# Optimization experiments

Measured on AMD Instinct MI355X. Metric: run time of the kernel, lower is better.

Reference implementation:

```python
import jax, jax.numpy as jnp
import numpy as np

IN_DIM = 512
HID = 256
SAMPLE = 8
TAU = 0.5
LAMBDA = 1.0
NUM_MLP = 3


def l2norm(x, axis=-1, eps=1e-12):
    n = jnp.sqrt(jnp.sum(x * x, axis=axis, keepdims=True))
    return x / jnp.maximum(n, eps)


def graphconv(adj, x, W, b):
    # GraphConv: aggregate then linear transform
    return adj @ (x @ W) + b


def mlp(x, Ws, bs):
    h = x
    for i in range(len(Ws) - 1):
        h = jax.nn.relu(h @ Ws[i] + bs[i])
    return h @ Ws[-1] + bs[-1]


def setup_inputs() -> dict:
    key = jax.random.key(0)
    ks = jax.random.split(key, 24)
    N = 16384
    # sparse-ish row-normalized adjacency surrogate (dense storage)
    a1 = jax.random.uniform(ks[0], (N, N), jnp.float32)
    a1 = (a1 > 0.999).astype(jnp.float32)
    adj1 = a1 / jnp.maximum(a1.sum(1, keepdims=True), 1.0)
    a2 = jax.random.uniform(ks[1], (N, N), jnp.float32)
    a2 = (a2 > 0.999).astype(jnp.float32)
    adj2 = a2 / jnp.maximum(a2.sum(1, keepdims=True), 1.0)
    x1 = jax.random.normal(ks[2], (N, IN_DIM), jnp.float32)
    x2 = jax.random.normal(ks[3], (N, IN_DIM), jnp.float32)
    neighbor_idx = jax.random.randint(ks[4], (N, SAMPLE), 0, N)
    neg_idx = jax.random.randint(ks[5], (N, SAMPLE), 0, N)

    def lin(k, fi, fo):
        k1, k2 = jax.random.split(k)
        s = 1.0 / np.sqrt(fi)
        return (jax.random.uniform(k1, (fi, fo), jnp.float32, -s, s),
                jax.random.uniform(k2, (fo,), jnp.float32, -s, s))

    W1, b1 = lin(ks[6], IN_DIM, HID)
    W2, b2 = lin(ks[7], HID, HID)
    tW1, tb1 = lin(ks[8], IN_DIM, HID)
    tW2, tb2 = lin(ks[9], HID, HID)
    projW, projB, semW, semB = [], [], [], []
    for i in range(NUM_MLP):
        w, b = lin(ks[10 + i], HID, HID)
        projW.append(w); projB.append(b)
        w, b = lin(ks[14 + i], HID, HID)
        semW.append(w); semB.append(b)
    return dict(adj1=adj1, adj2=adj2, x1=x1, x2=x2,
                neighbor_idx=neighbor_idx, neg_idx=neg_idx,
                W1=W1, b1=b1, W2=W2, b2=b2,
                tW1=tW1, tb1=tb1, tW2=tW2, tb2=tb2,
                projW0=projW[0], projB0=projB[0], projW1=projW[1], projB1=projB[1], projW2=projW[2], projB2=projB[2],
                semW0=semW[0], semB0=semB[0], semW1=semW[1], semB1=semB[1], semW2=semW[2], semB2=semB[2])


def contrastive_loss(projected_emd, v_emd, samp_u, samp_neg_v):
    # projected_emd, v_emd: [N,1,D]; samp_u, samp_neg_v: [N,S,D]
    pos = jnp.exp(jnp.einsum('nod,nsd->ns', projected_emd, samp_u) / TAU)  # [N,S]
    neg_sum = jnp.sum(jnp.exp(jnp.einsum('nod,nsd->ns', v_emd, samp_neg_v) / TAU), axis=1)  # [N]
    neg_score = jnp.sum(jnp.log(pos + neg_sum[:, None]), axis=1)  # [N]
    pos_score = jnp.sum(jnp.log(pos), axis=1)
    total = jnp.sum(LAMBDA * neg_score - pos_score)
    return total / samp_u.shape[0] / samp_u.shape[1]


def semi_loss(z1, z2):
    z1n = l2norm(z1); z2n = l2norm(z2)
    refl = jnp.exp((z1n @ z1n.T) / TAU)      # [N,N]
    between = jnp.exp((z1n @ z2n.T) / TAU)   # [N,N]
    return -jnp.log(jnp.diagonal(between) / (refl.sum(1) + between.sum(1) - jnp.diagonal(refl)))


def reference(adj1, adj2, x1, x2, neighbor_idx, neg_idx,
              W1, b1, W2, b2, tW1, tb1, tW2, tb2,
              projW0, projB0, projW1, projB1, projW2, projB2,
              semW0, semB0, semW1, semB1, semW2, semB2):
    pW = [projW0, projW1, projW2]; pB = [projB0, projB1, projB2]
    sW = [semW0, semW1, semW2]; sB = [semB0, semB1, semB2]
    h1 = graphconv(adj1, x1, W1, b1)
    h2 = graphconv(adj1, x2, W1, b1)
    h3 = graphconv(adj2, graphconv(adj2, x1, W1, b1), W2, b2)  # v_emd
    u_emd = l2norm(graphconv(adj2, graphconv(adj2, x1, tW1, tb1), tW2, tb2))
    projected = l2norm(mlp(h3, pW, pB))
    h1_proj = l2norm(mlp(h1, sW, sB))
    h2_proj = l2norm(mlp(h2, sW, sB))

    v_norm = l2norm(h3)
    samp_u = u_emd[neighbor_idx]          # [N,S,D]
    samp_neg_v = v_norm[neg_idx]          # [N,S,D]
    gacl = contrastive_loss(projected[:, None, :], v_norm[:, None, :], samp_u, samp_neg_v)

    l1 = semi_loss(h1_proj, h2_proj)
    l2 = semi_loss(h2_proj, h1_proj)
    sem = jnp.mean((l1 + l2) * 0.5)

    total = gacl + 0.6 * sem
    return total, gacl, sem, h3
```

## Files before the change

kernel.cpp:

```cpp
#include <hip/hip_runtime.h>
#include <hip/hip_bf16.h>

#define NN   16384
#define IND  512
#define HID  256
#define SAMP 8
#define CAP  64

typedef __bf16 bf16;
typedef __bf16 bf16x4 __attribute__((ext_vector_type(4)));
typedef __bf16 bf16x8 __attribute__((ext_vector_type(8)));
typedef float  f32x4  __attribute__((ext_vector_type(4)));

#define LOG2E_2 2.8853900817779268f

#define GLOAD_LDS16(gptr, lptr) \
  __builtin_amdgcn_global_load_lds((const __attribute__((address_space(1))) void*)(gptr), \
                                   (__attribute__((address_space(3))) void*)(lptr), 16, 0, 0)

__global__ void cvt_x(const float* __restrict__ a, bf16* __restrict__ oa,
                      const float* __restrict__ b, bf16* __restrict__ ob) {
  const float* src = blockIdx.y ? b : a;
  bf16* dst = blockIdx.y ? ob : oa;
  int stride = gridDim.x * blockDim.x;
  for (int i = blockIdx.x * blockDim.x + threadIdx.x; i < (NN * IND) / 4; i += stride) {
    float4 v = ((const float4*)src)[i];
    bf16x4 o = {(bf16)v.x, (bf16)v.y, (bf16)v.z, (bf16)v.w};
    *(bf16x4*)(dst + (size_t)i * 4) = o;
  }
}

struct WtArgs {
  const float* src[10];
  bf16* dst[10];
  int K[10];
};

__global__ void cvt_weights(WtArgs a) {
  int w = blockIdx.y;
  int K = a.K[w];
  int total = K * HID;
  const float* s = a.src[w];
  bf16* d = a.dst[w];
  for (int i = blockIdx.x * blockDim.x + threadIdx.x; i < total; i += gridDim.x * blockDim.x) {
    int k = i >> 8, n = i & 255;
    d[n * K + k] = (bf16)s[i];
  }
}

__global__ void scan_adj(const float* __restrict__ adjA, const float* __restrict__ adjB,
                         int* __restrict__ colsA, int* __restrict__ cntA,
                         int* __restrict__ colsB, int* __restrict__ cntB) {
  const float* adj = blockIdx.y ? adjB : adjA;
  int* cols = blockIdx.y ? colsB : colsA;
  int* cnt = blockIdx.y ? cntB : cntA;
  int r = blockIdx.x;
  __shared__ int c;
  if (threadIdx.x == 0) c = 0;
  __syncthreads();
  const float4* row = (const float4*)(adj + (size_t)r * NN);
  int* rc = cols + (size_t)r * CAP;
  #pragma unroll 4
  for (int i = threadIdx.x; i < NN / 4; i += 256) {
    float4 v = row[i];
    if (v.x != 0.f || v.y != 0.f || v.z != 0.f || v.w != 0.f) {
      if (v.x != 0.f) { int p = atomicAdd(&c, 1); if (p < CAP) rc[p] = 4 * i; }
      if (v.y != 0.f) { int p = atomicAdd(&c, 1); if (p < CAP) rc[p] = 4 * i + 1; }
      if (v.z != 0.f) { int p = atomicAdd(&c, 1); if (p < CAP) rc[p] = 4 * i + 2; }
      if (v.w != 0.f) { int p = atomicAdd(&c, 1); if (p < CAP) rc[p] = 4 * i + 3; }
    }
  }
  __syncthreads();
  if (threadIdx.x == 0) cnt[r] = (c < CAP) ? c : CAP;
}

struct SpmmB {
  const int* cols[4]; const int* cnt[4]; const float* X[4]; const float* bias[4];
  float* outF[4];
  bf16* outB[4];
  float* outNF[4];
};
__global__ void spmm_b(SpmmB s) {
  int j = blockIdx.y;
  int wid = threadIdx.x >> 6, lane = threadIdx.x & 63;
  int r = blockIdx.x * 4 + wid;
  int c = s.cnt[j][r];
  float val = 1.0f / (float)(c > 0 ? c : 1);
  const int* rc = s.cols[j] + (size_t)r * CAP;
  const float* X = s.X[j];
  float ax = 0.f, ay = 0.f, az = 0.f, aw = 0.f;
  for (int t = 0; t < c; ++t) {
    int col = rc[t];
    float4 v = ((const float4*)(X + (size_t)col * HID))[lane];
    ax += v.x; ay += v.y; az += v.z; aw += v.w;
  }
  float4 b4 = ((const float4*)s.bias[j])[lane];
  ax = ax * val + b4.x; ay = ay * val + b4.y; az = az * val + b4.z; aw = aw * val + b4.w;
  if (s.outF[j]) {
    float* o = s.outF[j] + (size_t)r * HID + lane * 4;
    o[0] = ax; o[1] = ay; o[2] = az; o[3] = aw;
  }
  if (s.outB[j]) {
    bf16x4 ob = {(bf16)ax, (bf16)ay, (bf16)az, (bf16)aw};
    *(bf16x4*)(s.outB[j] + (size_t)r * HID + lane * 4) = ob;
  }
  if (s.outNF[j]) {
    float ss = ax * ax + ay * ay + az * az + aw * aw;
    #pragma unroll
    for (int off = 1; off < 64; off <<= 1) ss += __shfl_xor(ss, off);
    float inv = 1.0f / fmaxf(sqrtf(ss), 1e-12f);
    float4 o = {ax * inv, ay * inv, az * inv, aw * inv};
    ((float4*)(s.outNF[j] + (size_t)r * HID))[lane] = o;
  }
}

struct GemmB {
  const bf16* A[3]; const bf16* Bt[3]; const float* bias[3];
  float* Cf[3]; bf16* Cb[3];
};
__global__ __launch_bounds__(256) void gemm_b(GemmB g, int K, int relu) {
  __shared__ bf16 As[128][64];
  __shared__ bf16 Bs[128][64];
  int j = blockIdx.z;
  const bf16* A = g.A[j];
  const bf16* Bt = g.Bt[j];
  int m0 = blockIdx.x * 128, n0 = blockIdx.y * 128;
  int tid = threadIdx.x, wid = tid >> 6, lane = tid & 63;
  int wm = wid >> 1, wn = wid & 1, q = lane >> 4, li = lane & 15;
  int r8 = lane >> 3, cc8 = lane & 7;
  int csw = cc8 ^ r8;
  f32x4 acc[4][4] = {};
  for (int k0 = 0; k0 < K; k0 += 64) {
    if (k0) __syncthreads();
    const bf16* gA = A + (size_t)(m0 + wid * 32 + r8) * K + k0 + csw * 8;
    const bf16* gB = Bt + (size_t)(n0 + wid * 32 + r8) * K + k0 + csw * 8;
    #pragma unroll
    for (int jj = 0; jj < 4; ++jj) {
      GLOAD_LDS16(gA + (size_t)jj * 8 * K, &As[wid * 32 + jj * 8][0]);
      GLOAD_LDS16(gB + (size_t)jj * 8 * K, &Bs[wid * 32 + jj * 8][0]);
    }
    __syncthreads();
    #pragma unroll
    for (int kk = 0; kk < 64; kk += 32) {
      int ca = (((q + (kk >> 3)) ^ (li & 7)) << 3);
      bf16x8 af[4], bfr[4];
      #pragma unroll
      for (int im = 0; im < 4; ++im) af[im] = *(const bf16x8*)(&As[wm * 64 + im * 16 + li][ca]);
      #pragma unroll
      for (int in = 0; in < 4; ++in) bfr[in] = *(const bf16x8*)(&Bs[wn * 64 + in * 16 + li][ca]);
      #pragma unroll
      for (int im = 0; im < 4; ++im)
        #pragma unroll
        for (int in = 0; in < 4; ++in)
          acc[im][in] = __builtin_amdgcn_mfma_f32_16x16x32_bf16(af[im], bfr[in], acc[im][in], 0, 0, 0);
    }
  }
  float* Cf = g.Cf[j];
  bf16* Cb = g.Cb[j];
  const float* bias = g.bias[j];
  #pragma unroll
  for (int im = 0; im < 4; ++im) {
    int grow0 = m0 + wm * 64 + im * 16 + q * 4;
    #pragma unroll
    for (int in = 0; in < 4; ++in) {
      int gcol = n0 + wn * 64 + in * 16 + li;
      float bv = bias ? bias[gcol] : 0.f;
      #pragma unroll
      for (int reg = 0; reg < 4; ++reg) {
        float v = acc[im][in][reg] + bv;
        if (relu) v = fmaxf(v, 0.f);
        size_t idx = (size_t)(grow0 + reg) * HID + gcol;
        if (Cf) Cf[idx] = v;
        if (Cb) Cb[idx] = (bf16)v;
      }
    }
  }
}

__global__ __launch_bounds__(128, 2) void flash_sem3(
    const bf16* __restrict__ P, const bf16* __restrict__ Q,
    float* __restrict__ Ra, float* __restrict__ Rb,
    float* __restrict__ Cr, float* __restrict__ Cc) {
  int z = blockIdx.z;
  int bid = blockIdx.y * 128 + blockIdx.x;
  int grp = bid >> 8, loc = bid & 255;
  int bx = (grp & 7) * 16 + (loc & 15);
  int by = (grp >> 3) * 16 + (loc >> 4);
  if (z < 2 && by < bx) return;
  const bf16* X = (z == 1) ? Q : P;
  const bf16* Y = (z == 0) ? P : Q;
  float* rowacc = (z == 0) ? Ra : (z == 1) ? Rb : Cr;
  float* colacc = (z == 2) ? Cc : rowacc;
  bool docol = (z == 2) || (bx != by);
  int m0 = bx * 128, n0 = by * 128;
  int wid = threadIdx.x >> 6, lane = threadIdx.x & 63;
  int q = lane >> 4, li = lane & 15;
  const bf16* Arow = X + (size_t)(m0 + wid * 64 + li) * HID + q * 8;
  const bf16* Brow = Y + (size_t)(n0 + li) * HID + q * 8;
  f32x4 acc[4][8] = {};
  #pragma unroll
  for (int kk = 0; kk < 8; ++kk) {
    bf16x8 af[4], bfr[8];
    #pragma unroll
    for (int im = 0; im < 4; ++im)
      af[im] = *(const bf16x8*)(Arow + (size_t)im * 16 * HID + kk * 32);
    #pragma unroll
    for (int in = 0; in < 8; ++in)
      bfr[in] = *(const bf16x8*)(Brow + (size_t)in * 16 * HID + kk * 32);
    #pragma unroll
    for (int im = 0; im < 4; ++im)
      #pragma unroll
      for (int in = 0; in < 8; ++in)
        acc[im][in] = __builtin_amdgcn_mfma_f32_16x16x32_bf16(af[im], bfr[in], acc[im][in], 0, 0, 0);
  }
  float cs[8] = {};
  #pragma unroll
  for (int im = 0; im < 4; ++im) {
    #pragma unroll
    for (int reg = 0; reg < 4; ++reg) {
      float rs = 0.f;
      #pragma unroll
      for (int in = 0; in < 8; ++in) {
        float e = exp2f(acc[im][in][reg] * LOG2E_2);
        rs += e;
        cs[in] += e;
      }
      rs += __shfl_xor(rs, 1); rs += __shfl_xor(rs, 2);
      rs += __shfl_xor(rs, 4); rs += __shfl_xor(rs, 8);
      if (li == 0) atomicAdd(&rowacc[m0 + wid * 64 + im * 16 + q * 4 + reg], rs);
    }
  }
  if (docol) {
    #pragma unroll
    for (int in = 0; in < 8; ++in) {
      float v = cs[in];
      v += __shfl_xor(v, 16); v += __shfl_xor(v, 32);
      if (q == 0) atomicAdd(&colacc[n0 + in * 16 + li], v);
    }
  }
}

struct NormB { const float* X[3]; float* outF[3]; bf16* outB[3]; };
__global__ void l2norm_b(NormB n) {
  int j = blockIdx.y;
  int wid = threadIdx.x >> 6, lane = threadIdx.x & 63;
  int r = blockIdx.x * 4 + wid;
  float4 a = ((const float4*)(n.X[j] + (size_t)r * HID))[lane];
  float s = a.x * a.x + a.y * a.y + a.z * a.z + a.w * a.w;
  #pragma unroll
  for (int off = 1; off < 64; off <<= 1) s += __shfl_xor(s, off);
  float inv = 1.0f / fmaxf(sqrtf(s), 1e-12f);
  a.x *= inv; a.y *= inv; a.z *= inv; a.w *= inv;
  if (n.outF[j]) ((float4*)(n.outF[j] + (size_t)r * HID))[lane] = a;
  if (n.outB[j]) {
    bf16x4 b = {(bf16)a.x, (bf16)a.y, (bf16)a.z, (bf16)a.w};
    *(bf16x4*)(n.outB[j] + (size_t)r * HID + lane * 4) = b;
  }
}

__global__ void tail_k(const float* __restrict__ proj, const float* __restrict__ vn,
                       const float* __restrict__ ue, const int* __restrict__ nbr,
                       const int* __restrict__ neg,
                       const float* __restrict__ P, const float* __restrict__ Q2,
                       const float* __restrict__ Ra, const float* __restrict__ Rb,
                       const float* __restrict__ Cr, const float* __restrict__ Cc,
                       float* __restrict__ sums) {
  int wid = threadIdx.x >> 6, lane = threadIdx.x & 63;
  int n = blockIdx.x * 4 + wid;
  if (blockIdx.y == 0) {
    float4 p = ((const float4*)(proj + (size_t)n * HID))[lane];
    float4 v = ((const float4*)(vn + (size_t)n * HID))[lane];
    float du[SAMP], dn[SAMP];
    for (int s = 0; s < SAMP; ++s) {
      int iu = nbr[n * SAMP + s];
      float4 u = ((const float4*)(ue + (size_t)iu * HID))[lane];
      float d = p.x * u.x + p.y * u.y + p.z * u.z + p.w * u.w;
      #pragma unroll
      for (int off = 1; off < 64; off <<= 1) d += __shfl_xor(d, off);
      du[s] = d;
      int iv = neg[n * SAMP + s];
      float4 w = ((const float4*)(vn + (size_t)iv * HID))[lane];
      float d2 = v.x * w.x + v.y * w.y + v.z * w.z + v.w * w.w;
      #pragma unroll
      for (int off = 1; off < 64; off <<= 1) d2 += __shfl_xor(d2, off);
      dn[s] = d2;
    }
    float negsum = 0.f;
    for (int s = 0; s < SAMP; ++s) negsum += expf(2.f * dn[s]);
    float ns = 0.f, ps = 0.f;
    for (int s = 0; s < SAMP; ++s) {
      float pl = 2.f * du[s];
      ns += logf(expf(pl) + negsum);
      ps += pl;
    }
    if (lane == 0) atomicAdd(&sums[0], ns - ps);
  } else {
    float4 a = ((const float4*)(P + (size_t)n * HID))[lane];
    float4 b = ((const float4*)(Q2 + (size_t)n * HID))[lane];
    float d = a.x * b.x + a.y * b.y + a.z * b.z + a.w * b.w;
    #pragma unroll
    for (int off = 1; off < 64; off <<= 1) d += __shfl_xor(d, off);
    float db = expf(2.f * d);
    float e2 = expf(2.f);
    float l1 = -logf(db / (Ra[n] + Cr[n] - e2));
    float l2 = -logf(db / (Rb[n] + Cc[n] - e2));
    if (lane == 0) atomicAdd(&sums[1], 0.5f * (l1 + l2));
  }
}

__global__ void final_k(const float* __restrict__ sums, float* __restrict__ out) {
  float gacl = sums[0] / (float)(NN * SAMP);
  float sem = sums[1] / (float)NN;
  out[0] = gacl + 0.6f * sem;
  out[1] = gacl;
  out[2] = sem;
}

extern "C" void kernel_launch(void* const* d_in, const int* in_sizes, int n_in,
                              void* d_out, int out_size, void* d_ws, size_t ws_size,
                              hipStream_t stream) {
  (void)in_sizes; (void)n_in; (void)out_size; (void)ws_size;
  const float* adj1 = (const float*)d_in[0];
  const float* adj2 = (const float*)d_in[1];
  const float* x1 = (const float*)d_in[2];
  const float* x2 = (const float*)d_in[3];
  const int* nbr = (const int*)d_in[4];
  const int* neg = (const int*)d_in[5];
  const float* W1 = (const float*)d_in[6];
  const float* b1 = (const float*)d_in[7];
  const float* W2 = (const float*)d_in[8];
  const float* b2 = (const float*)d_in[9];
  const float* tW1 = (const float*)d_in[10];
  const float* tb1 = (const float*)d_in[11];
  const float* tW2 = (const float*)d_in[12];
  const float* tb2 = (const float*)d_in[13];
  const float* pB[3] = {(const float*)d_in[15], (const float*)d_in[17], (const float*)d_in[19]};
  const float* sB[3] = {(const float*)d_in[21], (const float*)d_in[23], (const float*)d_in[25]};

  char* w = (char*)d_ws;
  auto alloc = [&](size_t bytes) -> char* {
    char* p = w;
    w += (bytes + 255) & ~(size_t)255;
    return p;
  };
  float* Ra = (float*)alloc((size_t)NN * 4);
  float* Rb = (float*)alloc((size_t)NN * 4);
  float* Cr = (float*)alloc((size_t)NN * 4);
  float* Cc = (float*)alloc((size_t)NN * 4);
  float* sums = (float*)alloc(256);
  size_t accBytes = (size_t)(w - (char*)d_ws);

  int* c1cols = (int*)alloc((size_t)NN * CAP * 4);
  int* c1cnt = (int*)alloc((size_t)NN * 4);
  int* c2cols = (int*)alloc((size_t)NN * CAP * 4);
  int* c2cnt = (int*)alloc((size_t)NN * 4);
  bf16* x1b = (bf16*)alloc((size_t)NN * IND * 2);
  bf16* x2b = (bf16*)alloc((size_t)NN * IND * 2);
  bf16* W1t = (bf16*)alloc((size_t)IND * HID * 2);
  bf16* tW1t = (bf16*)alloc((size_t)IND * HID * 2);
  bf16* W2t = (bf16*)alloc((size_t)HID * HID * 2);
  bf16* tW2t = (bf16*)alloc((size_t)HID * HID * 2);
  bf16* pWt[3], *sWt[3];
  for (int i = 0; i < 3; ++i) pWt[i] = (bf16*)alloc((size_t)HID * HID * 2);
  for (int i = 0; i < 3; ++i) sWt[i] = (bf16*)alloc((size_t)HID * HID * 2);
  const size_t FB = (size_t)NN * HID * 4;
  float* xw1 = (float*)alloc(FB);
  float* xw2 = (float*)alloc(FB);
  float* xt1 = (float*)alloc(FB);
  float* mlp_out = (float*)alloc(FB);
  float* projected = (float*)alloc(FB);
  float* h1p = (float*)alloc(FB);
  float* h2p = (float*)alloc(FB);
  float* v_norm = (float*)alloc(FB);
  float* gw = xw2;
  float* utw = xt1;
  float* u_emd = xw1;
  const size_t BB = (size_t)NN * HID * 2;
  bf16* h1b = (bf16*)alloc(BB);
  bf16* h2b = (bf16*)alloc(BB);
  bf16* gb = (bf16*)alloc(BB);
  bf16* h3b = (bf16*)alloc(BB);
  bf16* utb = (bf16*)alloc(BB);
  bf16* mA = (bf16*)alloc(BB);
  bf16* mB = (bf16*)alloc(BB);
  bf16* mB1 = x1b;
  bf16* mB2 = x1b + (size_t)NN * HID;
  bf16* Pb = gb;
  bf16* Qb = utb;

  hipMemsetAsync(d_ws, 0, accBytes, stream);

  WtArgs wa;
  const float* wsrc[10] = {W1, tW1, W2, tW2,
                           (const float*)d_in[14], (const float*)d_in[16], (const float*)d_in[18],
                           (const float*)d_in[20], (const float*)d_in[22], (const float*)d_in[24]};
  bf16* wdst[10] = {W1t, tW1t, W2t, tW2t, pWt[0], pWt[1], pWt[2], sWt[0], sWt[1], sWt[2]};
  int wk[10] = {IND, IND, HID, HID, HID, HID, HID, HID, HID, HID};
  for (int i = 0; i < 10; ++i) { wa.src[i] = wsrc[i]; wa.dst[i] = wdst[i]; wa.K[i] = wk[i]; }
  cvt_weights<<<dim3(512, 10), 256, 0, stream>>>(wa);
  cvt_x<<<dim3(2048, 2), 256, 0, stream>>>(x1, x1b, x2, x2b);
  scan_adj<<<dim3(NN, 2), 256, 0, stream>>>(adj1, adj2, c1cols, c1cnt, c2cols, c2cnt);

  {
    GemmB g = {};
    g.A[0] = x1b; g.Bt[0] = W1t; g.Cf[0] = xw1;
    g.A[1] = x2b; g.Bt[1] = W1t; g.Cf[1] = xw2;
    g.A[2] = x1b; g.Bt[2] = tW1t; g.Cf[2] = xt1;
    gemm_b<<<dim3(128, 2, 3), 256, 0, stream>>>(g, IND, 0);
  }
  {
    SpmmB s = {};
    s.cols[0] = c1cols; s.cnt[0] = c1cnt; s.X[0] = xw1; s.bias[0] = b1; s.outB[0] = h1b;
    s.cols[1] = c1cols; s.cnt[1] = c1cnt; s.X[1] = xw2; s.bias[1] = b1; s.outB[1] = h2b;
    s.cols[2] = c2cols; s.cnt[2] = c2cnt; s.X[2] = xw1; s.bias[2] = b1; s.outB[2] = gb;
    s.cols[3] = c2cols; s.cnt[3] = c2cnt; s.X[3] = xt1; s.bias[3] = tb1; s.outB[3] = utb;
    spmm_b<<<dim3(NN / 4, 4), 256, 0, stream>>>(s);
  }
  {
    GemmB g = {};
    g.A[0] = gb; g.Bt[0] = W2t; g.Cf[0] = gw;
    g.A[1] = utb; g.Bt[1] = tW2t; g.Cf[1] = utw;
    gemm_b<<<dim3(128, 2, 2), 256, 0, stream>>>(g, HID, 0);
  }
  float* h3out = ((float*)d_out) + 3;
  {
    SpmmB s = {};
    s.cols[0] = c2cols; s.cnt[0] = c2cnt; s.X[0] = gw; s.bias[0] = b2;
    s.outF[0] = h3out; s.outB[0] = h3b; s.outNF[0] = v_norm;
    s.cols[1] = c2cols; s.cnt[1] = c2cnt; s.X[1] = utw; s.bias[1] = tb2;
    s.outNF[1] = u_emd;
    spmm_b<<<dim3(NN / 4, 2), 256, 0, stream>>>(s);
  }
  {
    GemmB g = {};
    g.A[0] = h3b; g.Bt[0] = pWt[0]; g.bias[0] = pB[0]; g.Cb[0] = mA;
    g.A[1] = h1b; g.Bt[1] = sWt[0]; g.bias[1] = sB[0]; g.Cb[1] = gb;
    g.A[2] = h2b; g.Bt[2] = sWt[0]; g.bias[2] = sB[0]; g.Cb[2] = utb;
    gemm_b<<<dim3(128, 2, 3), 256, 0, stream>>>(g, HID, 1);
  }
  {
    GemmB g = {};
    g.A[0] = mA; g.Bt[0] = pWt[1]; g.bias[0] = pB[1]; g.Cb[0] = mB;
    g.A[1] = gb; g.Bt[1] = sWt[1]; g.bias[1] = sB[1]; g.Cb[1] = mB1;
    g.A[2] = utb; g.Bt[2] = sWt[1]; g.bias[2] = sB[1]; g.Cb[2] = mB2;
    gemm_b<<<dim3(128, 2, 3), 256, 0, stream>>>(g, HID, 1);
  }
  {
    GemmB g = {};
    g.A[0] = mB; g.Bt[0] = pWt[2]; g.bias[0] = pB[2]; g.Cf[0] = mlp_out;
    g.A[1] = mB1; g.Bt[1] = sWt[2]; g.bias[1] = sB[2]; g.Cf[1] = xw2;
    g.A[2] = mB2; g.Bt[2] = sWt[2]; g.bias[2] = sB[2]; g.Cf[2] = xt1;
    gemm_b<<<dim3(128, 2, 3), 256, 0, stream>>>(g, HID, 0);
  }
  {
    NormB nb2 = {};
    nb2.X[0] = mlp_out; nb2.outF[0] = projected;
    nb2.X[1] = xw2; nb2.outF[1] = h1p; nb2.outB[1] = Pb;
    nb2.X[2] = xt1; nb2.outF[2] = h2p; nb2.outB[2] = Qb;
    l2norm_b<<<dim3(NN / 4, 3), 256, 0, stream>>>(nb2);
  }

  flash_sem3<<<dim3(128, 128, 3), 128, 0, stream>>>(Pb, Qb, Ra, Rb, Cr, Cc);
  tail_k<<<dim3(NN / 4, 2), 256, 0, stream>>>(projected, v_norm, u_emd, nbr, neg,
                                              h1p, h2p, Ra, Rb, Cr, Cc, sums);
  final_k<<<1, 1, 0, stream>>>(sums, (float*)d_out);
}
```

Measured before the change: 3.614 ms.

## Stage sim tiles in swizzled LDS and split across four waves

The similarity/exp kernel now loads the full 128x256 A and B tiles into shared memory with direct global-to-LDS loads, using an XOR swizzle to avoid bank conflicts. Before, each wave read its operands straight from global memory, and each B row was fetched by multiple waves. The block grows to 256 threads in a 2x2 wave grid, so each wave computes a 64x64 sub-tile and holds fewer accumulators. The cost is 128KB of LDS per block, which allows one block per CU and no overlap between the load phase and the compute phase.

```diff
diff --git a/kernel.cpp b/kernel.cpp
--- a/kernel.cpp
+++ b/kernel.cpp
@@ -177,10 +177,12 @@
   }
 }
 
-__global__ __launch_bounds__(128, 2) void flash_sem3(
+__global__ __launch_bounds__(256, 1) void flash_sem4(
     const bf16* __restrict__ P, const bf16* __restrict__ Q,
     float* __restrict__ Ra, float* __restrict__ Rb,
     float* __restrict__ Cr, float* __restrict__ Cc) {
+  __shared__ bf16 As[128][256];
+  __shared__ bf16 Bs[128][256];
   int z = blockIdx.z;
   int bid = blockIdx.y * 128 + blockIdx.x;
   int grp = bid >> 8, loc = bid & 255;
@@ -193,49 +195,60 @@
   float* colacc = (z == 2) ? Cc : rowacc;
   bool docol = (z == 2) || (bx != by);
   int m0 = bx * 128, n0 = by * 128;
-  int wid = threadIdx.x >> 6, lane = threadIdx.x & 63;
-  int q = lane >> 4, li = lane & 15;
-  const bf16* Arow = X + (size_t)(m0 + wid * 64 + li) * HID + q * 8;
-  const bf16* Brow = Y + (size_t)(n0 + li) * HID + q * 8;
-  f32x4 acc[4][8] = {};
+  int tid = threadIdx.x, wid = tid >> 6, lane = tid & 63;
+  int wm = wid >> 1, wn = wid & 1, q = lane >> 4, li = lane & 15;
+  int r2 = lane >> 5, c32 = lane & 31;
   #pragma unroll
-  for (int kk = 0; kk < 8; ++kk) {
-    bf16x8 af[4], bfr[8];
+  for (int i = 0; i < 16; ++i) {
+    int rl = wid * 32 + i * 2 + r2;
+    int csrc = c32 ^ (rl & 31);
+    GLOAD_LDS16(X + (size_t)(m0 + rl) * HID + csrc * 8, &As[wid * 32 + i * 2][0]);
+    GLOAD_LDS16(Y + (size_t)(n0 + rl) * HID + csrc * 8, &Bs[wid * 32 + i * 2][0]);
+  }
+  __syncthreads();
+  f32x4 acc[4][4] = {};
+  #pragma unroll
+  for (int k = 0; k < 8; ++k) {
+    bf16x8 af[4], bfr[4];
+    #pragma unroll
+    for (int im = 0; im < 4; ++im) {
+      int row = wm * 64 + im * 16 + li;
+      af[im] = *(const bf16x8*)(&As[row][(((k * 4 + q) ^ (row & 31)) << 3)]);
+    }
+    #pragma unroll
+    for (int in = 0; in < 4; ++in) {
+      int row = wn * 64 + in * 16 + li;
+      bfr[in] = *(const bf16x8*)(&Bs[row][(((k * 4 + q) ^ (row & 31)) << 3)]);
+    }
     #pragma unroll
     for (int im = 0; im < 4; ++im)
-      af[im] = *(const bf16x8*)(Arow + (size_t)im * 16 * HID + kk * 32);
-    #pragma unroll
-    for (int in = 0; in < 8; ++in)
-      bfr[in] = *(const bf16x8*)(Brow + (size_t)in * 16 * HID + kk * 32);
-    #pragma unroll
-    for (int im = 0; im < 4; ++im)
-      #pragma unroll
-      for (int in = 0; in < 8; ++in)
+      #pragma unroll
+      for (int in = 0; in < 4; ++in)
         acc[im][in] = __builtin_amdgcn_mfma_f32_16x16x32_bf16(af[im], bfr[in], acc[im][in], 0, 0, 0);
   }
-  float cs[8] = {};
+  float cs[4] = {0.f, 0.f, 0.f, 0.f};
   #pragma unroll
   for (int im = 0; im < 4; ++im) {
     #pragma unroll
     for (int reg = 0; reg < 4; ++reg) {
       float rs = 0.f;
       #pragma unroll
-      for (int in = 0; in < 8; ++in) {
+      for (int in = 0; in < 4; ++in) {
         float e = exp2f(acc[im][in][reg] * LOG2E_2);
         rs += e;
         cs[in] += e;
       }
       rs += __shfl_xor(rs, 1); rs += __shfl_xor(rs, 2);
       rs += __shfl_xor(rs, 4); rs += __shfl_xor(rs, 8);
-      if (li == 0) atomicAdd(&rowacc[m0 + wid * 64 + im * 16 + q * 4 + reg], rs);
+      if (li == 0) atomicAdd(&rowacc[m0 + wm * 64 + im * 16 + q * 4 + reg], rs);
     }
   }
   if (docol) {
     #pragma unroll
-    for (int in = 0; in < 8; ++in) {
+    for (int in = 0; in < 4; ++in) {
       float v = cs[in];
       v += __shfl_xor(v, 16); v += __shfl_xor(v, 32);
-      if (q == 0) atomicAdd(&colacc[n0 + in * 16 + li], v);
+      if (q == 0) atomicAdd(&colacc[n0 + wn * 64 + in * 16 + li], v);
     }
   }
 }
@@ -460,7 +473,7 @@
     l2norm_b<<<dim3(NN / 4, 3), 256, 0, stream>>>(nb2);
   }
 
-  flash_sem3<<<dim3(128, 128, 3), 128, 0, stream>>>(Pb, Qb, Ra, Rb, Cr, Cc);
+  flash_sem4<<<dim3(128, 128, 3), 256, 0, stream>>>(Pb, Qb, Ra, Rb, Cr, Cc);
   tail_k<<<dim3(NN / 4, 2), 256, 0, stream>>>(projected, v_norm, u_emd, nbr, neg,
                                               h1p, h2p, Ra, Rb, Cr, Cc, sums);
   final_k<<<1, 1, 0, stream>>>(sums, (float*)d_out);
```

Result: slower. 3.737 ms (+3.4%).

## Restructure semantic-loss kernel with register-resident column tiles and LDS-staged rows

Applied to the files above, without the earlier changes.

The semantic similarity kernel changes from 128x128 output tiles with symmetric skipping and row/column atomics to a layout where each wave holds 128 columns of B fragments in registers. Blocks stream half of the rows through double-buffered, XOR-swizzled LDS using global_load_lds, and accumulate only column sums, giving four launches in place of three symmetric ones. Separately, the intermediate XW products feeding the sparse aggregation are stored in bf16 rather than fp32, halving gather traffic. The trade-offs are that the symmetry saving is lost (more MFMA work), registers are heavily used by 64 fragments per thread, and precision drops in the aggregations.

```diff
diff --git a/kernel.cpp b/kernel.cpp
--- a/kernel.cpp
+++ b/kernel.cpp
@@ -75,7 +75,7 @@
 }
 
 struct SpmmB {
-  const int* cols[4]; const int* cnt[4]; const float* X[4]; const float* bias[4];
+  const int* cols[4]; const int* cnt[4]; const bf16* X[4]; const float* bias[4];
   float* outF[4];
   bf16* outB[4];
   float* outNF[4];
@@ -87,12 +87,12 @@
   int c = s.cnt[j][r];
   float val = 1.0f / (float)(c > 0 ? c : 1);
   const int* rc = s.cols[j] + (size_t)r * CAP;
-  const float* X = s.X[j];
+  const bf16* X = s.X[j];
   float ax = 0.f, ay = 0.f, az = 0.f, aw = 0.f;
   for (int t = 0; t < c; ++t) {
     int col = rc[t];
-    float4 v = ((const float4*)(X + (size_t)col * HID))[lane];
-    ax += v.x; ay += v.y; az += v.z; aw += v.w;
+    bf16x4 v = *(const bf16x4*)(X + (size_t)col * HID + lane * 4);
+    ax += (float)v[0]; ay += (float)v[1]; az += (float)v[2]; aw += (float)v[3];
   }
   float4 b4 = ((const float4*)s.bias[j])[lane];
   ax = ax * val + b4.x; ay = ay * val + b4.y; az = az * val + b4.z; aw = aw * val + b4.w;
@@ -177,66 +177,77 @@
   }
 }
 
-__global__ __launch_bounds__(128, 2) void flash_sem3(
+__global__ __launch_bounds__(256, 1) void flash_sem5(
     const bf16* __restrict__ P, const bf16* __restrict__ Q,
     float* __restrict__ Ra, float* __restrict__ Rb,
     float* __restrict__ Cr, float* __restrict__ Cc) {
+  __shared__ bf16 As[2][128 * 256];
   int z = blockIdx.z;
-  int bid = blockIdx.y * 128 + blockIdx.x;
-  int grp = bid >> 8, loc = bid & 255;
-  int bx = (grp & 7) * 16 + (loc & 15);
-  int by = (grp >> 3) * 16 + (loc >> 4);
-  if (z < 2 && by < bx) return;
-  const bf16* X = (z == 1) ? Q : P;
-  const bf16* Y = (z == 0) ? P : Q;
-  float* rowacc = (z == 0) ? Ra : (z == 1) ? Rb : Cr;
-  float* colacc = (z == 2) ? Cc : rowacc;
-  bool docol = (z == 2) || (bx != by);
-  int m0 = bx * 128, n0 = by * 128;
-  int wid = threadIdx.x >> 6, lane = threadIdx.x & 63;
+  const bf16 *X, *Y;
+  float* out;
+  if (z == 0)      { X = P; Y = P; out = Ra; }
+  else if (z == 1) { X = Q; Y = Q; out = Rb; }
+  else if (z == 2) { X = P; Y = Q; out = Cc; }
+  else             { X = Q; Y = P; out = Cr; }
+  int tid = threadIdx.x, wid = tid >> 6, lane = tid & 63;
   int q = lane >> 4, li = lane & 15;
-  const bf16* Arow = X + (size_t)(m0 + wid * 64 + li) * HID + q * 8;
-  const bf16* Brow = Y + (size_t)(n0 + li) * HID + q * 8;
-  f32x4 acc[4][8] = {};
+  int cbase = blockIdx.x * 512 + wid * 128;
+  bf16x8 bfrag[8][8];
   #pragma unroll
-  for (int kk = 0; kk < 8; ++kk) {
-    bf16x8 af[4], bfr[8];
-    #pragma unroll
-    for (int im = 0; im < 4; ++im)
-      af[im] = *(const bf16x8*)(Arow + (size_t)im * 16 * HID + kk * 32);
-    #pragma unroll
-    for (int in = 0; in < 8; ++in)
-      bfr[in] = *(const bf16x8*)(Brow + (size_t)in * 16 * HID + kk * 32);
-    #pragma unroll
-    for (int im = 0; im < 4; ++im)
+  for (int in = 0; in < 8; ++in) {
+    const bf16* Yr = Y + (size_t)(cbase + in * 16 + li) * HID + q * 8;
+    #pragma unroll
+    for (int kk = 0; kk < 8; ++kk)
+      bfrag[in][kk] = *(const bf16x8*)(Yr + kk * 32);
+  }
+  float cs[8] = {};
+  int i0 = blockIdx.y * (NN / 2);
+  int l5 = lane >> 5, cp = lane & 31;
+  auto stage = [&](int chunk, int b) {
+    const bf16* src = X + (size_t)(i0 + chunk * 128) * HID;
+    #pragma unroll
+    for (int n = 0; n < 16; ++n) {
+      int idx = wid * 16 + n;
+      int r = idx * 2 + l5;
+      int csrc = cp ^ (r & 31);
+      GLOAD_LDS16(src + (size_t)r * HID + csrc * 8, &As[b][idx * 512]);
+    }
+  };
+  stage(0, 0);
+  __syncthreads();
+  for (int c = 0; c < 64; ++c) {
+    int b = c & 1;
+    if (c + 1 < 64) stage(c + 1, b ^ 1);
+    const bf16* buf = &As[b][0];
+    #pragma unroll
+    for (int ii = 0; ii < 8; ++ii) {
+      bf16x8 af[8];
+      #pragma unroll
+      for (int kk = 0; kk < 8; ++kk) {
+        int r = ii * 16 + li;
+        int c16 = (kk * 4 + q) ^ (r & 31);
+        af[kk] = *(const bf16x8*)(buf + r * 256 + c16 * 8);
+      }
+      f32x4 acc[8] = {};
+      #pragma unroll
+      for (int kk = 0; kk < 8; ++kk)
+        #pragma unroll
+        for (int in = 0; in < 8; ++in)
+          acc[in] = __builtin_amdgcn_mfma_f32_16x16x32_bf16(af[kk], bfrag[in][kk], acc[in], 0, 0, 0);
       #pragma unroll
       for (int in = 0; in < 8; ++in)
-        acc[im][in] = __builtin_amdgcn_mfma_f32_16x16x32_bf16(af[im], bfr[in], acc[im][in], 0, 0, 0);
-  }
-  float cs[8] = {};
+        #pragma unroll
+        for (int reg = 0; reg < 4; ++reg)
+          cs[in] += exp2f(acc[in][reg] * LOG2E_2);
+    }
+    __syncthreads();
+  }
   #pragma unroll
-  for (int im = 0; im < 4; ++im) {
-    #pragma unroll
-    for (int reg = 0; reg < 4; ++reg) {
-      float rs = 0.f;
-      #pragma unroll
-      for (int in = 0; in < 8; ++in) {
-        float e = exp2f(acc[im][in][reg] * LOG2E_2);
-        rs += e;
-        cs[in] += e;
-      }
-      rs += __shfl_xor(rs, 1); rs += __shfl_xor(rs, 2);
-      rs += __shfl_xor(rs, 4); rs += __shfl_xor(rs, 8);
-      if (li == 0) atomicAdd(&rowacc[m0 + wid * 64 + im * 16 + q * 4 + reg], rs);
-    }
-  }
-  if (docol) {
-    #pragma unroll
-    for (int in = 0; in < 8; ++in) {
-      float v = cs[in];
-      v += __shfl_xor(v, 16); v += __shfl_xor(v, 32);
-      if (q == 0) atomicAdd(&colacc[n0 + in * 16 + li], v);
-    }
+  for (int in = 0; in < 8; ++in) {
+    float v = cs[in];
+    v += __shfl_xor(v, 16);
+    v += __shfl_xor(v, 32);
+    if (q == 0) atomicAdd(&out[cbase + in * 16 + li], v);
   }
 }
 
@@ -363,30 +374,32 @@
   bf16* pWt[3], *sWt[3];
   for (int i = 0; i < 3; ++i) pWt[i] = (bf16*)alloc((size_t)HID * HID * 2);
   for (int i = 0; i < 3; ++i) sWt[i] = (bf16*)alloc((size_t)HID * HID * 2);
-  const size_t FB = (size_t)NN * HID * 4;
-  float* xw1 = (float*)alloc(FB);
-  float* xw2 = (float*)alloc(FB);
-  float* xt1 = (float*)alloc(FB);
-  float* mlp_out = (float*)alloc(FB);
-  float* projected = (float*)alloc(FB);
-  float* h1p = (float*)alloc(FB);
-  float* h2p = (float*)alloc(FB);
-  float* v_norm = (float*)alloc(FB);
-  float* gw = xw2;
-  float* utw = xt1;
-  float* u_emd = xw1;
   const size_t BB = (size_t)NN * HID * 2;
+  bf16* xw1b = (bf16*)alloc(BB);
+  bf16* xw2b = (bf16*)alloc(BB);
+  bf16* xt1b = (bf16*)alloc(BB);
+  bf16* gwb = (bf16*)alloc(BB);
+  bf16* utwb = (bf16*)alloc(BB);
   bf16* h1b = (bf16*)alloc(BB);
   bf16* h2b = (bf16*)alloc(BB);
-  bf16* gb = (bf16*)alloc(BB);
+  bf16* gb_ = (bf16*)alloc(BB);
   bf16* h3b = (bf16*)alloc(BB);
   bf16* utb = (bf16*)alloc(BB);
   bf16* mA = (bf16*)alloc(BB);
   bf16* mB = (bf16*)alloc(BB);
-  bf16* mB1 = x1b;
-  bf16* mB2 = x1b + (size_t)NN * HID;
-  bf16* Pb = gb;
-  bf16* Qb = utb;
+  bf16* mB1 = (bf16*)alloc(BB);
+  bf16* mB2 = (bf16*)alloc(BB);
+  bf16* Pb = (bf16*)alloc(BB);
+  bf16* Qb = (bf16*)alloc(BB);
+  const size_t FB = (size_t)NN * HID * 4;
+  float* u_emd = (float*)alloc(FB);
+  float* v_norm = (float*)alloc(FB);
+  float* projected = (float*)alloc(FB);
+  float* h1p = (float*)alloc(FB);
+  float* h2p = (float*)alloc(FB);
+  float* mlp_out = (float*)alloc(FB);
+  float* s3a = (float*)alloc(FB);
+  float* s3b = (float*)alloc(FB);
 
   hipMemsetAsync(d_ws, 0, accBytes, stream);
 
@@ -403,64 +416,64 @@
 
   {
     GemmB g = {};
-    g.A[0] = x1b; g.Bt[0] = W1t; g.Cf[0] = xw1;
-    g.A[1] = x2b; g.Bt[1] = W1t; g.Cf[1] = xw2;
-    g.A[2] = x1b; g.Bt[2] = tW1t; g.Cf[2] = xt1;
+    g.A[0] = x1b; g.Bt[0] = W1t; g.Cb[0] = xw1b;
+    g.A[1] = x2b; g.Bt[1] = W1t; g.Cb[1] = xw2b;
+    g.A[2] = x1b; g.Bt[2] = tW1t; g.Cb[2] = xt1b;
     gemm_b<<<dim3(128, 2, 3), 256, 0, stream>>>(g, IND, 0);
   }
   {
     SpmmB s = {};
-    s.cols[0] = c1cols; s.cnt[0] = c1cnt; s.X[0] = xw1; s.bias[0] = b1; s.outB[0] = h1b;
-    s.cols[1] = c1cols; s.cnt[1] = c1cnt; s.X[1] = xw2; s.bias[1] = b1; s.outB[1] = h2b;
-    s.cols[2] = c2cols; s.cnt[2] = c2cnt; s.X[2] = xw1; s.bias[2] = b1; s.outB[2] = gb;
-    s.cols[3] = c2cols; s.cnt[3] = c2cnt; s.X[3] = xt1; s.bias[3] = tb1; s.outB[3] = utb;
+    s.cols[0] = c1cols; s.cnt[0] = c1cnt; s.X[0] = xw1b; s.bias[0] = b1; s.outB[0] = h1b;
+    s.cols[1] = c1cols; s.cnt[1] = c1cnt; s.X[1] = xw2b; s.bias[1] = b1; s.outB[1] = h2b;
+    s.cols[2] = c2cols; s.cnt[2] = c2cnt; s.X[2] = xw1b; s.bias[2] = b1; s.outB[2] = gb_;
+    s.cols[3] = c2cols; s.cnt[3] = c2cnt; s.X[3] = xt1b; s.bias[3] = tb1; s.outB[3] = utb;
     spmm_b<<<dim3(NN / 4, 4), 256, 0, stream>>>(s);
   }
   {
     GemmB g = {};
-    g.A[0] = gb; g.Bt[0] = W2t; g.Cf[0] = gw;
-    g.A[1] = utb; g.Bt[1] = tW2t; g.Cf[1] = utw;
+    g.A[0] = gb_; g.Bt[0] = W2t; g.Cb[0] = gwb;
+    g.A[1] = utb; g.Bt[1] = tW2t; g.Cb[1] = utwb;
     gemm_b<<<dim3(128, 2, 2), 256, 0, stream>>>(g, HID, 0);
   }
   float* h3out = ((float*)d_out) + 3;
   {
     SpmmB s = {};
-    s.cols[0] = c2cols; s.cnt[0] = c2cnt; s.X[0] = gw; s.bias[0] = b2;
+    s.cols[0] = c2cols; s.cnt[0] = c2cnt; s.X[0] = gwb; s.bias[0] = b2;
     s.outF[0] = h3out; s.outB[0] = h3b; s.outNF[0] = v_norm;
-    s.cols[1] = c2cols; s.cnt[1] = c2cnt; s.X[1] = utw; s.bias[1] = tb2;
+    s.cols[1] = c2cols; s.cnt[1] = c2cnt; s.X[1] = utwb; s.bias[1] = tb2;
     s.outNF[1] = u_emd;
     spmm_b<<<dim3(NN / 4, 2), 256, 0, stream>>>(s);
   }
   {
     GemmB g = {};
     g.A[0] = h3b; g.Bt[0] = pWt[0]; g.bias[0] = pB[0]; g.Cb[0] = mA;
-    g.A[1] = h1b; g.Bt[1] = sWt[0]; g.bias[1] = sB[0]; g.Cb[1] = gb;
+    g.A[1] = h1b; g.Bt[1] = sWt[0]; g.bias[1] = sB[0]; g.Cb[1] = gb_;
     g.A[2] = h2b; g.Bt[2] = sWt[0]; g.bias[2] = sB[0]; g.Cb[2] = utb;
     gemm_b<<<dim3(128, 2, 3), 256, 0, stream>>>(g, HID, 1);
   }
   {
     GemmB g = {};
     g.A[0] = mA; g.Bt[0] = pWt[1]; g.bias[0] = pB[1]; g.Cb[0] = mB;
-    g.A[1] = gb; g.Bt[1] = sWt[1]; g.bias[1] = sB[1]; g.Cb[1] = mB1;
+    g.A[1] = gb_; g.Bt[1] = sWt[1]; g.bias[1] = sB[1]; g.Cb[1] = mB1;
     g.A[2] = utb; g.Bt[2] = sWt[1]; g.bias[2] = sB[1]; g.Cb[2] = mB2;
     gemm_b<<<dim3(128, 2, 3), 256, 0, stream>>>(g, HID, 1);
   }
   {
     GemmB g = {};
     g.A[0] = mB; g.Bt[0] = pWt[2]; g.bias[0] = pB[2]; g.Cf[0] = mlp_out;
-    g.A[1] = mB1; g.Bt[1] = sWt[2]; g.bias[1] = sB[2]; g.Cf[1] = xw2;
-    g.A[2] = mB2; g.Bt[2] = sWt[2]; g.bias[2] = sB[2]; g.Cf[2] = xt1;
+    g.A[1] = mB1; g.Bt[1] = sWt[2]; g.bias[1] = sB[2]; g.Cf[1] = s3a;
+    g.A[2] = mB2; g.Bt[2] = sWt[2]; g.bias[2] = sB[2]; g.Cf[2] = s3b;
     gemm_b<<<dim3(128, 2, 3), 256, 0, stream>>>(g, HID, 0);
   }
   {
     NormB nb2 = {};
     nb2.X[0] = mlp_out; nb2.outF[0] = projected;
-    nb2.X[1] = xw2; nb2.outF[1] = h1p; nb2.outB[1] = Pb;
-    nb2.X[2] = xt1; nb2.outF[2] = h2p; nb2.outB[2] = Qb;
+    nb2.X[1] = s3a; nb2.outF[1] = h1p; nb2.outB[1] = Pb;
+    nb2.X[2] = s3b; nb2.outF[2] = h2p; nb2.outB[2] = Qb;
     l2norm_b<<<dim3(NN / 4, 3), 256, 0, stream>>>(nb2);
   }
 
-  flash_sem3<<<dim3(128, 128, 3), 128, 0, stream>>>(Pb, Qb, Ra, Rb, Cr, Cc);
+  flash_sem5<<<dim3(32, 2, 4), 256, 0, stream>>>(Pb, Qb, Ra, Rb, Cr, Cc);
   tail_k<<<dim3(NN / 4, 2), 256, 0, stream>>>(projected, v_norm, u_emd, nbr, neg,
                                               h1p, h2p, Ra, Rb, Cr, Cc, sums);
   final_k<<<1, 1, 0, stream>>>(sums, (float*)d_out);
```

Result: slower. 3.723 ms (+3.0%).
